# Kernel optimization log

Hardware: AMD Instinct MI355X
Metric: run time of the kernel (lower is better)

## Reference

```python
import math
import jax, jax.numpy as jnp
import numpy as np

B, S, D, H = 2, 2048, 1024, 16
HD = D // H  # head_dim = 64


def setup_inputs() -> dict:
    key = jax.random.key(0)
    k1, k2, k3 = jax.random.split(key, 3)
    scale = 0.02
    return {
        "x": jax.random.normal(k1, (B, S, D), dtype=jnp.float32),
        "w_qkv": jax.random.normal(k2, (D, 3 * D), dtype=jnp.float32) * scale,
        "b_qkv": jnp.zeros((3 * D,), dtype=jnp.float32),
        "w_proj": jax.random.normal(k3, (D, D), dtype=jnp.float32) * scale,
        "b_proj": jnp.zeros((D,), dtype=jnp.float32),
    }


def reference(x, w_qkv, b_qkv, w_proj, b_proj):
    bsz, seq_len, d_model = x.shape
    # fused qkv projection: [B,S,3D] -> [3,B,H,S,HD]
    qkv = (x @ w_qkv + b_qkv).reshape(bsz, seq_len, 3, H, HD)
    qkv = jnp.transpose(qkv, (2, 0, 3, 1, 4))
    q, k, v = qkv[0], qkv[1], qkv[2]
    # scores [B,H,S,S]
    scores = jnp.einsum("bhqd,bhkd->bhqk", q, k) / math.sqrt(HD)
    causal = jnp.tril(jnp.ones((seq_len, seq_len), dtype=bool))
    scores = jnp.where(causal[None, None], scores, -jnp.inf)
    probs = jax.nn.softmax(scores, axis=-1)
    # dropout = 0.0 (eval mode)
    context = jnp.einsum("bhqk,bhkd->bhqd", probs, v)
    context = jnp.transpose(context, (0, 2, 1, 3)).reshape(bsz, seq_len, d_model)
    return context @ w_proj + b_proj
```

## Files before the change

### kernel.cpp

```cpp
#include <hip/hip_runtime.h>

#define B_ 2
#define S_ 2048
#define D_ 1024
#define H_ 16
#define HD_ 64
#define M_ (B_*S_)
#define N_QKV (3*D_)

typedef __attribute__((ext_vector_type(8))) short short8;
typedef __attribute__((ext_vector_type(4))) float floatx4;

__device__ __forceinline__ float fast_exp2(float x) {
    return __builtin_amdgcn_exp2f(x);
}

__device__ __forceinline__ unsigned short f2b(float f) {
    union { float f; unsigned int u; } v; v.f = f;
    unsigned int u = v.u;
    u += 0x7FFFu + ((u >> 16) & 1u);
    return (unsigned short)(u >> 16);
}
__device__ __forceinline__ unsigned short f2b_fast(float f) {
    union { float f; unsigned int u; } v; v.f = f;
    return (unsigned short)((v.u + 0x8000u) >> 16);
}

__device__ __forceinline__ void glds16(const unsigned short* g, unsigned short* lds) {
    __builtin_amdgcn_global_load_lds(
        (const __attribute__((address_space(1))) unsigned int*)g,
        (__attribute__((address_space(3))) unsigned int*)lds, 16, 0, 0);
}

__global__ void cast_bf16_kernel(const float* __restrict__ src,
                                 unsigned short* __restrict__ dst, int n) {
    int i = (blockIdx.x * blockDim.x + threadIdx.x) * 4;
    if (i >= n) return;
    float4 f = *(const float4*)(src + i);
    ushort4 o;
    o.x = f2b(f.x); o.y = f2b(f.y); o.z = f2b(f.z); o.w = f2b(f.w);
    *(ushort4*)(dst + i) = o;
}

__global__ void transpose_cast_kernel(const float* __restrict__ W,
                                      unsigned short* __restrict__ Wt,
                                      int rows, int cols) {
    __shared__ float tile[32][33];
    int c0 = blockIdx.x * 32, r0 = blockIdx.y * 32;
    int tx = threadIdx.x, ty = threadIdx.y;
    #pragma unroll
    for (int i = 0; i < 4; ++i)
        tile[ty + i*8][tx] = W[(size_t)(r0 + ty + i*8) * cols + c0 + tx];
    __syncthreads();
    #pragma unroll
    for (int i = 0; i < 4; ++i)
        Wt[(size_t)(c0 + ty + i*8) * rows + r0 + tx] = f2b(tile[tx][ty + i*8]);
}

__global__ __launch_bounds__(256, 3) void gemm_bt_kernel(
    const unsigned short* __restrict__ A,
    const unsigned short* __restrict__ Bt,
    const float* __restrict__ bias,
    unsigned short* __restrict__ q,
    unsigned short* __restrict__ k_,
    unsigned short* __restrict__ vt,
    int Kdim)
{
    __shared__ unsigned short As[128*64];
    __shared__ unsigned short Bs[128*64];

    const int t = threadIdx.x;
    const int lane = t & 63;
    const int w = t >> 6;
    const int wm = w >> 1, wn = w & 1;
    const int quad = lane >> 4, l15 = lane & 15;
    const int bm = blockIdx.y, bn = blockIdx.x;

    const int sr32 = t >> 3;
    const int gch  = (t & 7) ^ (sr32 & 7);

    const unsigned short* gA = A  + (size_t)(bm*128 + sr32) * Kdim + gch*8;
    const unsigned short* gB = Bt + (size_t)(bn*128 + sr32) * Kdim + gch*8;
    const size_t rstep = (size_t)32 * Kdim;

    unsigned short* lA = As + (w*8)*64;
    unsigned short* lB = Bs + (w*8)*64;

    const int swz = (l15 & 7);

    floatx4 acc[4][4];
    #pragma unroll
    for (int i = 0; i < 4; ++i)
        #pragma unroll
        for (int j = 0; j < 4; ++j)
            acc[i][j] = (floatx4){0.f, 0.f, 0.f, 0.f};

    for (int k0 = 0; k0 < Kdim; k0 += 64) {
        #pragma unroll
        for (int c = 0; c < 4; ++c) {
            glds16(gA + c*rstep + k0, lA + c*2048);
            glds16(gB + c*rstep + k0, lB + c*2048);
        }
        __syncthreads();
        short8 an[4][2], am[4][2];
        #pragma unroll
        for (int i = 0; i < 4; ++i)
            #pragma unroll
            for (int kk = 0; kk < 2; ++kk) {
                const int coff = ((quad + 4*kk) ^ swz) * 8;
                an[i][kk] = *(const short8*)&Bs[(wn*64 + i*16 + l15)*64 + coff];
                am[i][kk] = *(const short8*)&As[(wm*64 + i*16 + l15)*64 + coff];
            }
        #pragma unroll
        for (int kk = 0; kk < 2; ++kk)
            #pragma unroll
            for (int i = 0; i < 4; ++i)
                #pragma unroll
                for (int j = 0; j < 4; ++j)
                    acc[i][j] = __builtin_amdgcn_mfma_f32_16x16x32_bf16(an[i][kk], am[j][kk], acc[i][j], 0, 0, 0);
        __syncthreads();
    }

    const float QSCALE = 0.18033688011112042f;
    const int which = bn >> 3;
    const int hcol  = (bn & 7)*2 + wn;
    const int b     = bm >> 4;
    const int sbase = (bm & 15)*128 + wm*64;

    #pragma unroll
    for (int i = 0; i < 4; ++i) {
        float4 bias4 = *(const float4*)&bias[bn*128 + wn*64 + i*16 + quad*4];
        const int hd0 = i*16 + quad*4;
        #pragma unroll
        for (int j = 0; j < 4; ++j) {
            const int srow = sbase + j*16 + l15;
            float v0 = acc[i][j][0] + bias4.x;
            float v1 = acc[i][j][1] + bias4.y;
            float v2 = acc[i][j][2] + bias4.z;
            float v3 = acc[i][j][3] + bias4.w;
            if (which == 0) {
                v0 *= QSCALE; v1 *= QSCALE; v2 *= QSCALE; v3 *= QSCALE;
                ushort4 o; o.x = f2b(v0); o.y = f2b(v1); o.z = f2b(v2); o.w = f2b(v3);
                *(ushort4*)&q[((size_t)(b*H_ + hcol) * S_ + srow) * HD_ + hd0] = o;
            } else if (which == 1) {
                ushort4 o; o.x = f2b(v0); o.y = f2b(v1); o.z = f2b(v2); o.w = f2b(v3);
                *(ushort4*)&k_[((size_t)(b*H_ + hcol) * S_ + srow) * HD_ + hd0] = o;
            } else {
                const size_t vb = (size_t)(b*H_ + hcol) * HD_ + hd0;
                vt[(vb + 0) * S_ + srow] = f2b(v0);
                vt[(vb + 1) * S_ + srow] = f2b(v1);
                vt[(vb + 2) * S_ + srow] = f2b(v2);
                vt[(vb + 3) * S_ + srow] = f2b(v3);
            }
        }
    }
}

__global__ __launch_bounds__(256, 2) void gemm_bt64_kernel(
    const unsigned short* __restrict__ A,
    const unsigned short* __restrict__ Bt,
    const float* __restrict__ bias,
    float* __restrict__ outf,
    int Ndim, int Kdim)
{
    __shared__ unsigned short As[128*64];
    __shared__ unsigned short Bs[64*64];

    const int t = threadIdx.x;
    const int lane = t & 63;
    const int w = t >> 6;
    const int quad = lane >> 4, l15 = lane & 15;
    const int bm = blockIdx.y, bn = blockIdx.x;

    const int sr32 = t >> 3;
    const int gch  = (t & 7) ^ (sr32 & 7);

    const unsigned short* gA = A  + (size_t)(bm*128 + sr32) * Kdim + gch*8;
    const unsigned short* gB = Bt + (size_t)(bn*64  + sr32) * Kdim + gch*8;
    const size_t rstep = (size_t)32 * Kdim;

    unsigned short* lA = As + (w*8)*64;
    unsigned short* lB = Bs + (w*8)*64;

    const int swz = (l15 & 7);

    floatx4 acc[4][2];
    #pragma unroll
    for (int i = 0; i < 4; ++i)
        #pragma unroll
        for (int j = 0; j < 2; ++j)
            acc[i][j] = (floatx4){0.f, 0.f, 0.f, 0.f};

    for (int k0 = 0; k0 < Kdim; k0 += 64) {
        #pragma unroll
        for (int c = 0; c < 4; ++c)
            glds16(gA + c*rstep + k0, lA + c*2048);
        #pragma unroll
        for (int c = 0; c < 2; ++c)
            glds16(gB + c*rstep + k0, lB + c*2048);
        __syncthreads();
        short8 an[4][2], am[2][2];
        #pragma unroll
        for (int kk = 0; kk < 2; ++kk) {
            const int coff = ((quad + 4*kk) ^ swz) * 8;
            #pragma unroll
            for (int i = 0; i < 4; ++i)
                an[i][kk] = *(const short8*)&Bs[(i*16 + l15)*64 + coff];
            #pragma unroll
            for (int j = 0; j < 2; ++j)
                am[j][kk] = *(const short8*)&As[(w*32 + j*16 + l15)*64 + coff];
        }
        #pragma unroll
        for (int kk = 0; kk < 2; ++kk)
            #pragma unroll
            for (int i = 0; i < 4; ++i)
                #pragma unroll
                for (int j = 0; j < 2; ++j)
                    acc[i][j] = __builtin_amdgcn_mfma_f32_16x16x32_bf16(an[i][kk], am[j][kk], acc[i][j], 0, 0, 0);
        __syncthreads();
    }

    #pragma unroll
    for (int i = 0; i < 4; ++i) {
        float4 bias4 = *(const float4*)&bias[bn*64 + i*16 + quad*4];
        #pragma unroll
        for (int j = 0; j < 2; ++j) {
            const int gm = bm*128 + w*32 + j*16 + l15;
            float4 o;
            o.x = acc[i][j][0] + bias4.x;
            o.y = acc[i][j][1] + bias4.y;
            o.z = acc[i][j][2] + bias4.z;
            o.w = acc[i][j][3] + bias4.w;
            *(float4*)&outf[(size_t)gm * Ndim + bn*64 + i*16 + quad*4] = o;
        }
    }
}

__global__ __launch_bounds__(256, 2) void attn_kernel(
    const unsigned short* __restrict__ Q,
    const unsigned short* __restrict__ K,
    const unsigned short* __restrict__ Vt,
    unsigned short* __restrict__ ctx)
{
    __shared__ unsigned short KVs[2][2][64*64];
    __shared__ unsigned short Pt[4][2][16][72];

    const int t = threadIdx.x;
    const int lane = t & 63, w = t >> 6;
    const int quad = lane >> 4, l15 = lane & 15;
    const int bh = blockIdx.x & 31;
    const int a  = blockIdx.x >> 5;
    const int Hc = 31 - a;
    const int Lc = a;

    const unsigned short* Qh  = Q  + (size_t)bh * S_ * HD_;
    const unsigned short* Kh  = K  + (size_t)bh * S_ * HD_;
    const unsigned short* Vth = Vt + (size_t)bh * HD_ * S_;

    const int sr = t >> 3, sc = t & 7;
    const int gch = sc ^ (sr & 7);

    auto stage = [&](int j, int d) {
        unsigned short* kb = &KVs[d][0][0];
        unsigned short* vb = &KVs[d][1][0];
        const unsigned short* gk = Kh  + (size_t)(j*64 + sr)*HD_ + gch*8;
        const unsigned short* gv = Vth + (size_t)sr*S_ + (size_t)j*64 + gch*8;
        glds16(gk,                  kb + (w*8)*64);
        glds16(gk + 32*HD_,         kb + (32 + w*8)*64);
        glds16(gv,                  vb + (w*8)*64);
        glds16(gv + (size_t)32*S_,  vb + (32 + w*8)*64);
    };

    const int qH = Hc*64 + w*16;
    const int qL = Lc*64 + w*16;

    short8 bqH[2], bqL[2];
    #pragma unroll
    for (int kk = 0; kk < 2; ++kk) {
        bqH[kk] = *(const short8*)&Qh[(size_t)(qH + l15)*HD_ + kk*32 + quad*8];
        bqL[kk] = *(const short8*)&Qh[(size_t)(qL + l15)*HD_ + kk*32 + quad*8];
    }

    floatx4 OH[4], OL[4];
    #pragma unroll
    for (int nb = 0; nb < 4; ++nb) {
        OH[nb] = (floatx4){0.f,0.f,0.f,0.f};
        OL[nb] = (floatx4){0.f,0.f,0.f,0.f};
    }
    float lH = 0.f, lL = 0.f;

    auto do_tile = [&](const short8 (&bq)[2], floatx4 (&O)[4], float& l_acc,
                       int qbase, bool diag, int j, int ps,
                       const short8 (&ak)[4][2], const short8 (&av)[4][2]) {
        float z[4][4];
        __builtin_amdgcn_s_setprio(1);
        #pragma unroll
        for (int nb = 0; nb < 4; ++nb) {
            floatx4 c = (floatx4){0.f,0.f,0.f,0.f};
            c = __builtin_amdgcn_mfma_f32_16x16x32_bf16(ak[nb][0], bq[0], c, 0,0,0);
            c = __builtin_amdgcn_mfma_f32_16x16x32_bf16(ak[nb][1], bq[1], c, 0,0,0);
            #pragma unroll
            for (int r = 0; r < 4; ++r) z[nb][r] = c[r];
        }
        __builtin_amdgcn_s_setprio(0);
        if (diag) {
            const int qg = qbase + l15, koff = j*64;
            #pragma unroll
            for (int nb = 0; nb < 4; ++nb)
                #pragma unroll
                for (int r = 0; r < 4; ++r)
                    if (koff + nb*16 + quad*4 + r > qg) z[nb][r] = -1e30f;
        }
        float rs = 0.f;
        #pragma unroll
        for (int nb = 0; nb < 4; ++nb) {
            float p0 = fast_exp2(z[nb][0]);
            float p1 = fast_exp2(z[nb][1]);
            float p2 = fast_exp2(z[nb][2]);
            float p3 = fast_exp2(z[nb][3]);
            rs += (p0 + p1) + (p2 + p3);
            ushort4 pk;
            pk.x = f2b_fast(p0); pk.y = f2b_fast(p1);
            pk.z = f2b_fast(p2); pk.w = f2b_fast(p3);
            *(ushort4*)&Pt[w][ps][l15][nb*16 + quad*4] = pk;
        }
        l_acc += rs;
        short8 bp0 = *(const short8*)&Pt[w][ps][l15][quad*8];
        short8 bp1 = *(const short8*)&Pt[w][ps][l15][32 + quad*8];
        __builtin_amdgcn_s_setprio(1);
        #pragma unroll
        for (int nb = 0; nb < 4; ++nb) {
            O[nb] = __builtin_amdgcn_mfma_f32_16x16x32_bf16(av[nb][0], bp0, O[nb], 0,0,0);
            O[nb] = __builtin_amdgcn_mfma_f32_16x16x32_bf16(av[nb][1], bp1, O[nb], 0,0,0);
        }
        __builtin_amdgcn_s_setprio(0);
    };

    stage(0, 0);

    for (int j = 0; j <= Hc; ++j) {
        __syncthreads();
        if (j < Hc) stage(j+1, (j+1)&1);
        const int d = j & 1;
        const unsigned short* Ksb = &KVs[d][0][0];
        const unsigned short* Vsb = &KVs[d][1][0];

        short8 ak[4][2], av[4][2];
        #pragma unroll
        for (int nb = 0; nb < 4; ++nb)
            #pragma unroll
            for (int kk = 0; kk < 2; ++kk) {
                int off = (nb*16 + l15)*64 + (((quad + 4*kk) ^ (l15 & 7)) * 8);
                ak[nb][kk] = *(const short8*)&Ksb[off];
                av[nb][kk] = *(const short8*)&Vsb[off];
            }

        do_tile(bqH, OH, lH, qH, j == Hc, j, 0, ak, av);
        if (j <= Lc)
            do_tile(bqL, OL, lL, qL, j == Lc, j, 1, ak, av);
    }

    const int b = bh >> 4, h = bh & (H_ - 1);
    auto finish = [&](floatx4 (&O)[4], float l_acc, int qbase) {
        l_acc += __shfl_xor(l_acc, 16, 64);
        l_acc += __shfl_xor(l_acc, 32, 64);
        const float inv = 1.f / l_acc;
        const int qg = qbase + l15;
        #pragma unroll
        for (int nb = 0; nb < 4; ++nb) {
            ushort4 o;
            o.x = f2b(O[nb][0] * inv);
            o.y = f2b(O[nb][1] * inv);
            o.z = f2b(O[nb][2] * inv);
            o.w = f2b(O[nb][3] * inv);
            *(ushort4*)&ctx[((size_t)(b*S_ + qg))*D_ + h*HD_ + nb*16 + quad*4] = o;
        }
    };
    finish(OH, lH, qH);
    finish(OL, lL, qL);
}

extern "C" void kernel_launch(void* const* d_in, const int* in_sizes, int n_in,
                              void* d_out, int out_size, void* d_ws, size_t ws_size,
                              hipStream_t stream) {
    const float* x      = (const float*)d_in[0];
    const float* w_qkv  = (const float*)d_in[1];
    const float* b_qkv  = (const float*)d_in[2];
    const float* w_proj = (const float*)d_in[3];
    const float* b_proj = (const float*)d_in[4];
    float* out = (float*)d_out;

    unsigned short* xb     = (unsigned short*)d_ws;
    unsigned short* wqkvT  = xb     + (size_t)M_ * D_;
    unsigned short* wprojT = wqkvT  + (size_t)N_QKV * D_;
    unsigned short* Qb     = wprojT + (size_t)D_ * D_;
    unsigned short* Kb     = Qb     + (size_t)B_*H_*S_*HD_;
    unsigned short* Vb     = Kb     + (size_t)B_*H_*S_*HD_;
    unsigned short* Vtb    = Vb     + (size_t)B_*H_*S_*HD_;
    unsigned short* ctx    = xb;

    cast_bf16_kernel<<<dim3((M_*D_/4 + 255)/256), dim3(256), 0, stream>>>(x, xb, M_*D_);
    transpose_cast_kernel<<<dim3(N_QKV/32, D_/32), dim3(32, 8), 0, stream>>>(w_qkv, wqkvT, D_, N_QKV);
    transpose_cast_kernel<<<dim3(D_/32, D_/32), dim3(32, 8), 0, stream>>>(w_proj, wprojT, D_, D_);

    gemm_bt_kernel<<<dim3(N_QKV/128, M_/128), dim3(256), 0, stream>>>(
        xb, wqkvT, b_qkv, Qb, Kb, Vtb, D_);

    attn_kernel<<<dim3(512), dim3(256), 0, stream>>>(Qb, Kb, Vtb, ctx);

    gemm_bt64_kernel<<<dim3(D_/64, M_/128), dim3(256), 0, stream>>>(
        ctx, wprojT, b_proj, out, D_, D_);
}
```

Baseline: 174.2 us.

## Overlap next K-tile global loads with MFMA and stage V-transpose through LDS

Both GEMM kernels now issue the global-to-LDS loads for the next K tile right after the current tile's fragments are read into registers. The second barrier moves before those loads, so the loads overlap the MFMA work instead of running serially before it. The V output of the QKV GEMM is transposed through padded shared memory and written as coalesced 16-byte rows instead of scattered 2-byte stores. This adds one LDS round trip and a barrier in the V epilogue, and enlarges shared memory slightly, which could affect occupancy at launch bounds of 3 blocks.

```diff
diff --git a/kernel.cpp b/kernel.cpp
--- a/kernel.cpp
+++ b/kernel.cpp
@@ -66,8 +66,9 @@
     unsigned short* __restrict__ vt,
     int Kdim)
 {
-    __shared__ unsigned short As[128*64];
-    __shared__ unsigned short Bs[128*64];
+    __shared__ unsigned short SMEM[128*136];
+    unsigned short* As = SMEM;
+    unsigned short* Bs = SMEM + 128*64;
 
     const int t = threadIdx.x;
     const int lane = t & 63;
@@ -88,6 +89,14 @@
 
     const int swz = (l15 & 7);
 
+    auto stage_g = [&](int kk) {
+        #pragma unroll
+        for (int c = 0; c < 4; ++c) {
+            glds16(gA + c*rstep + kk, lA + c*2048);
+            glds16(gB + c*rstep + kk, lB + c*2048);
+        }
+    };
+
     floatx4 acc[4][4];
     #pragma unroll
     for (int i = 0; i < 4; ++i)
@@ -95,12 +104,8 @@
         for (int j = 0; j < 4; ++j)
             acc[i][j] = (floatx4){0.f, 0.f, 0.f, 0.f};
 
+    stage_g(0);
     for (int k0 = 0; k0 < Kdim; k0 += 64) {
-        #pragma unroll
-        for (int c = 0; c < 4; ++c) {
-            glds16(gA + c*rstep + k0, lA + c*2048);
-            glds16(gB + c*rstep + k0, lB + c*2048);
-        }
         __syncthreads();
         short8 an[4][2], am[4][2];
         #pragma unroll
@@ -111,6 +116,8 @@
                 an[i][kk] = *(const short8*)&Bs[(wn*64 + i*16 + l15)*64 + coff];
                 am[i][kk] = *(const short8*)&As[(wm*64 + i*16 + l15)*64 + coff];
             }
+        __syncthreads();
+        if (k0 + 64 < Kdim) stage_g(k0 + 64);
         #pragma unroll
         for (int kk = 0; kk < 2; ++kk)
             #pragma unroll
@@ -118,39 +125,59 @@
                 #pragma unroll
                 for (int j = 0; j < 4; ++j)
                     acc[i][j] = __builtin_amdgcn_mfma_f32_16x16x32_bf16(an[i][kk], am[j][kk], acc[i][j], 0, 0, 0);
-        __syncthreads();
     }
 
     const float QSCALE = 0.18033688011112042f;
     const int which = bn >> 3;
     const int hcol  = (bn & 7)*2 + wn;
     const int b     = bm >> 4;
-    const int sbase = (bm & 15)*128 + wm*64;
-
-    #pragma unroll
-    for (int i = 0; i < 4; ++i) {
-        float4 bias4 = *(const float4*)&bias[bn*128 + wn*64 + i*16 + quad*4];
-        const int hd0 = i*16 + quad*4;
-        #pragma unroll
-        for (int j = 0; j < 4; ++j) {
-            const int srow = sbase + j*16 + l15;
-            float v0 = acc[i][j][0] + bias4.x;
-            float v1 = acc[i][j][1] + bias4.y;
-            float v2 = acc[i][j][2] + bias4.z;
-            float v3 = acc[i][j][3] + bias4.w;
-            if (which == 0) {
-                v0 *= QSCALE; v1 *= QSCALE; v2 *= QSCALE; v3 *= QSCALE;
-                ushort4 o; o.x = f2b(v0); o.y = f2b(v1); o.z = f2b(v2); o.w = f2b(v3);
-                *(ushort4*)&q[((size_t)(b*H_ + hcol) * S_ + srow) * HD_ + hd0] = o;
-            } else if (which == 1) {
-                ushort4 o; o.x = f2b(v0); o.y = f2b(v1); o.z = f2b(v2); o.w = f2b(v3);
-                *(ushort4*)&k_[((size_t)(b*H_ + hcol) * S_ + srow) * HD_ + hd0] = o;
-            } else {
-                const size_t vb = (size_t)(b*H_ + hcol) * HD_ + hd0;
-                vt[(vb + 0) * S_ + srow] = f2b(v0);
-                vt[(vb + 1) * S_ + srow] = f2b(v1);
-                vt[(vb + 2) * S_ + srow] = f2b(v2);
-                vt[(vb + 3) * S_ + srow] = f2b(v3);
+    const int sbase0 = (bm & 15)*128;
+    const int sbase  = sbase0 + wm*64;
+
+    if (which == 2) {
+        unsigned short (*L)[136] = (unsigned short (*)[136])SMEM;
+        #pragma unroll
+        for (int i = 0; i < 4; ++i) {
+            float4 bias4 = *(const float4*)&bias[bn*128 + wn*64 + i*16 + quad*4];
+            const int n0 = wn*64 + i*16 + quad*4;
+            #pragma unroll
+            for (int j = 0; j < 4; ++j) {
+                const int m = wm*64 + j*16 + l15;
+                L[n0+0][m] = f2b(acc[i][j][0] + bias4.x);
+                L[n0+1][m] = f2b(acc[i][j][1] + bias4.y);
+                L[n0+2][m] = f2b(acc[i][j][2] + bias4.z);
+                L[n0+3][m] = f2b(acc[i][j][3] + bias4.w);
+            }
+        }
+        __syncthreads();
+        const int r = t >> 1, half = t & 1;
+        const int hcr = (bn & 7)*2 + (r >> 6);
+        const int hdr = r & 63;
+        unsigned short* dst = &vt[(((size_t)(b*H_ + hcr))*HD_ + hdr)*S_ + sbase0 + half*64];
+        const unsigned short* srcL = &L[r][half*64];
+        #pragma unroll
+        for (int c = 0; c < 8; ++c)
+            *(uint4*)&dst[c*8] = *(const uint4*)&srcL[c*8];
+    } else {
+        #pragma unroll
+        for (int i = 0; i < 4; ++i) {
+            float4 bias4 = *(const float4*)&bias[bn*128 + wn*64 + i*16 + quad*4];
+            const int hd0 = i*16 + quad*4;
+            #pragma unroll
+            for (int j = 0; j < 4; ++j) {
+                const int srow = sbase + j*16 + l15;
+                float v0 = acc[i][j][0] + bias4.x;
+                float v1 = acc[i][j][1] + bias4.y;
+                float v2 = acc[i][j][2] + bias4.z;
+                float v3 = acc[i][j][3] + bias4.w;
+                if (which == 0) {
+                    v0 *= QSCALE; v1 *= QSCALE; v2 *= QSCALE; v3 *= QSCALE;
+                    ushort4 o; o.x = f2b(v0); o.y = f2b(v1); o.z = f2b(v2); o.w = f2b(v3);
+                    *(ushort4*)&q[((size_t)(b*H_ + hcol) * S_ + srow) * HD_ + hd0] = o;
+                } else {
+                    ushort4 o; o.x = f2b(v0); o.y = f2b(v1); o.z = f2b(v2); o.w = f2b(v3);
+                    *(ushort4*)&k_[((size_t)(b*H_ + hcol) * S_ + srow) * HD_ + hd0] = o;
+                }
             }
         }
     }
@@ -184,6 +211,15 @@
 
     const int swz = (l15 & 7);
 
+    auto stage_g = [&](int kk) {
+        #pragma unroll
+        for (int c = 0; c < 4; ++c)
+            glds16(gA + c*rstep + kk, lA + c*2048);
+        #pragma unroll
+        for (int c = 0; c < 2; ++c)
+            glds16(gB + c*rstep + kk, lB + c*2048);
+    };
+
     floatx4 acc[4][2];
     #pragma unroll
     for (int i = 0; i < 4; ++i)
@@ -191,13 +227,8 @@
         for (int j = 0; j < 2; ++j)
             acc[i][j] = (floatx4){0.f, 0.f, 0.f, 0.f};
 
+    stage_g(0);
     for (int k0 = 0; k0 < Kdim; k0 += 64) {
-        #pragma unroll
-        for (int c = 0; c < 4; ++c)
-            glds16(gA + c*rstep + k0, lA + c*2048);
-        #pragma unroll
-        for (int c = 0; c < 2; ++c)
-            glds16(gB + c*rstep + k0, lB + c*2048);
         __syncthreads();
         short8 an[4][2], am[2][2];
         #pragma unroll
@@ -210,6 +241,8 @@
             for (int j = 0; j < 2; ++j)
                 am[j][kk] = *(const short8*)&As[(w*32 + j*16 + l15)*64 + coff];
         }
+        __syncthreads();
+        if (k0 + 64 < Kdim) stage_g(k0 + 64);
         #pragma unroll
         for (int kk = 0; kk < 2; ++kk)
             #pragma unroll
@@ -217,7 +250,6 @@
                 #pragma unroll
                 for (int j = 0; j < 2; ++j)
                     acc[i][j] = __builtin_amdgcn_mfma_f32_16x16x32_bf16(an[i][kk], am[j][kk], acc[i][j], 0, 0, 0);
-        __syncthreads();
     }
 
     #pragma unroll
```

Measured after the change: 172.3 us (median of 2 runs). About the same (-1.1%).
